# Performance work log

Measured on AMD Instinct MI355X. Metric: run time of the kernel, lower is better.

The kernel has to match this reference:

```python
import jax, jax.numpy as jnp
import numpy as np

PH = PW = 5  # roi_size
EPS = 1e-5


def _conv1x1(x, w, b):
    # x: (B,Cin,H,W), w: (Cout,Cin)
    return jnp.einsum('bchw,oc->bohw', x, w) + b[None, :, None, None]


def _resize_ac(x, oh, ow):
    # F.interpolate bilinear, align_corners=True. x: (B,C,H,W)
    B, C, H, W = x.shape
    ys = jnp.linspace(0.0, H - 1.0, oh)
    xs = jnp.linspace(0.0, W - 1.0, ow)
    y0 = jnp.floor(ys).astype(jnp.int32); y1 = jnp.minimum(y0 + 1, H - 1)
    x0 = jnp.floor(xs).astype(jnp.int32); x1 = jnp.minimum(x0 + 1, W - 1)
    ly = (ys - y0)[:, None]; lx = (xs - x0)[None, :]
    v00 = x[:, :, y0[:, None], x0[None, :]]
    v01 = x[:, :, y0[:, None], x1[None, :]]
    v10 = x[:, :, y1[:, None], x0[None, :]]
    v11 = x[:, :, y1[:, None], x1[None, :]]
    return v00 * (1 - ly) * (1 - lx) + v01 * (1 - ly) * lx + v10 * ly * (1 - lx) + v11 * ly * lx


def _roi_align_one(feat, box):
    # torchvision RoIAlign, spatial_scale=1, sampling_ratio=1, aligned=False
    # feat: (C,H,W), box: (x1,y1,x2,y2)
    C, H, W = feat.shape
    bx1, by1, bx2, by2 = box[0], box[1], box[2], box[3]
    rw = jnp.maximum(bx2 - bx1, 1.0)
    rh = jnp.maximum(by2 - by1, 1.0)
    xs = bx1 + (jnp.arange(PW, dtype=feat.dtype) + 0.5) * (rw / PW)
    ys = by1 + (jnp.arange(PH, dtype=feat.dtype) + 0.5) * (rh / PH)
    yg = jnp.broadcast_to(ys[:, None], (PH, PW))
    xg = jnp.broadcast_to(xs[None, :], (PH, PW))
    valid = (yg >= -1.0) & (yg <= H) & (xg >= -1.0) & (xg <= W)
    y = jnp.clip(yg, 0.0, H - 1.0); x = jnp.clip(xg, 0.0, W - 1.0)
    y0 = jnp.floor(y).astype(jnp.int32); x0 = jnp.floor(x).astype(jnp.int32)
    y1i = jnp.minimum(y0 + 1, H - 1); x1i = jnp.minimum(x0 + 1, W - 1)
    ly = y - y0; lx = x - x0
    v = (feat[:, y0, x0] * (1 - ly) * (1 - lx) + feat[:, y0, x1i] * (1 - ly) * lx
         + feat[:, y1i, x0] * ly * (1 - lx) + feat[:, y1i, x1i] * ly * lx)
    return v * valid  # (C,PH,PW)


def _layernorm(x, w, b):
    mu = jnp.mean(x, -1, keepdims=True)
    var = jnp.var(x, -1, keepdims=True)
    return (x - mu) * jax.lax.rsqrt(var + EPS) * w + b


def setup_inputs() -> dict:
    key = jax.random.key(0)
    ks = jax.random.split(key, 16)
    B, G, NB, HF = 8, 8, 16, 28
    x4 = jax.random.normal(ks[0], (B, 1024, 14, 14), jnp.float32)
    x5 = jax.random.normal(ks[1], (B, 2048, 7, 7), jnp.float32)
    bx = jax.random.uniform(ks[2], (B, NB), minval=0.0, maxval=18.0)
    by = jax.random.uniform(ks[3], (B, NB), minval=0.0, maxval=18.0)
    bw = jax.random.uniform(ks[4], (B, NB), minval=3.0, maxval=10.0)
    bh = jax.random.uniform(ks[5], (B, NB), minval=3.0, maxval=10.0)
    boxes = jnp.stack([bx, by, jnp.minimum(bx + bw, 28.0), jnp.minimum(by + bh, 28.0)], -1)
    group = jax.random.randint(ks[6], (B, G, 2), 0, NB, jnp.int32)
    real_in_num = jnp.full((B,), G, jnp.int32)
    label_s = jax.random.randint(ks[7], (B, G), 0, 6, jnp.int64)
    label_s = jnp.where(jnp.arange(G)[None, :] % 3 == 0, -1, label_s)  # exercise both branches
    skeleton = jax.random.normal(ks[8], (B, G, HF, HF), jnp.float32)
    D = 1536 * PH * PW  # 38400
    return {
        'x4': x4, 'x5': x5, 'boxes': boxes, 'skeleton': skeleton,
        'group': group, 'real_in_num': real_in_num, 'label_s': label_s,
        'conv1_w': jax.random.normal(ks[9], (), jnp.float32) * 0.5,
        'conv1_b': jax.random.normal(ks[10], (), jnp.float32) * 0.1,
        'conv2_w': jax.random.normal(ks[11], (512, 1024), jnp.float32) * 0.03,
        'conv2_b': jnp.zeros((512,), jnp.float32),
        'conv3_w': jax.random.normal(ks[12], (1024, 2048), jnp.float32) * 0.02,
        'conv3_b': jnp.zeros((1024,), jnp.float32),
        'norm1_w': jnp.ones((D,), jnp.float32), 'norm1_b': jnp.zeros((D,), jnp.float32),
        'norm2_w': jnp.ones((512,), jnp.float32), 'norm2_b': jnp.zeros((512,), jnp.float32),
        'fc1_w': jax.random.normal(ks[13], (512, D), jnp.float32) * float(np.sqrt(2.0 / D)),
        'fc1_b': jnp.zeros((512,), jnp.float32),
        'fc2_w': jax.random.normal(ks[14], (6, 512), jnp.float32) * float(np.sqrt(2.0 / 512)),
        'fc2_b': jnp.zeros((6,), jnp.float32),
    }


def reference(x4, x5, boxes, skeleton, group, real_in_num, label_s,
              conv1_w, conv1_b, conv2_w, conv2_b, conv3_w, conv3_b,
              norm1_w, norm1_b, norm2_w, norm2_b, fc1_w, fc1_b, fc2_w, fc2_b):
    B, G = skeleton.shape[0], skeleton.shape[1]
    HF, WF = skeleton.shape[2], skeleton.shape[3]
    # backbone heads: 1x1 conv + bilinear upsample (align_corners=True), concat
    f4 = _resize_ac(_conv1x1(x4, conv2_w, conv2_b), HF, WF)   # (B,512,28,28)
    f5 = _resize_ac(_conv1x1(x5, conv3_w, conv3_b), HF, WF)   # (B,1024,28,28)
    app = jnp.concatenate([f4, f5], axis=1)                   # (B,1536,28,28)
    C = app.shape[1]
    # per-person pose gate: 1x1 conv (scalar on single channel) + sigmoid
    gate = jax.nn.sigmoid(skeleton * conv1_w + conv1_b)       # (B,G,28,28)
    gated = gate[:, :, None] * app[:, None]                   # (B,G,C,28,28)
    use_gate = (label_s != -1)[:, :, None, None, None]
    pose_feature = jnp.where(use_gate, gated, app[:, None])   # (B,G,C,28,28)
    # union box of the two interacting people (get_box_tensor)
    bidx = jnp.arange(B)[:, None]
    b1 = boxes[bidx, group[..., 0]]                           # (B,G,4)
    b2 = boxes[bidx, group[..., 1]]
    ub = jnp.stack([jnp.minimum(b1[..., 0], b2[..., 0]), jnp.minimum(b1[..., 1], b2[..., 1]),
                    jnp.maximum(b1[..., 2], b2[..., 2]), jnp.maximum(b1[..., 3], b2[..., 3])], -1)
    # batched RoIAlign over all N = B*G boxes
    feats = pose_feature.reshape(B * G, C, HF, WF)
    rois = jax.vmap(_roi_align_one)(feats, ub.reshape(B * G, 4))  # (N,C,5,5)
    sk = rois.reshape(B * G, -1)                              # (N,38400)
    sk = jax.nn.relu(_layernorm(sk, norm1_w, norm1_b))
    # dropout(p=0.9) is identity in eval mode
    sk = sk @ fc1_w.T + fc1_b
    sk = _layernorm(sk, norm2_w, norm2_b)
    score = sk @ fc2_w.T + fc2_b                              # (N,6)
    return score
```

## Files before the change

kernel.cpp:

```cpp
#include <hip/hip_runtime.h>
#include <hip/hip_cooperative_groups.h>
#include <math.h>

namespace cg = cooperative_groups;

#define B8   8
#define HW4  196
#define HW5  49
#define HFW  28
#define NPIX 784
#define CAPP 1536
#define D1   38400
#define NR   64

typedef short short8 __attribute__((ext_vector_type(8)));
typedef short short4v __attribute__((ext_vector_type(4)));
typedef float floatx16 __attribute__((ext_vector_type(16)));

__device__ __forceinline__ unsigned short f2bf(float f) {
  unsigned u = __float_as_uint(f);
  u += 0x7FFF + ((u >> 16) & 1);
  return (unsigned short)(u >> 16);
}

struct Params {
  const float *x4, *x5, *boxes, *skel;
  const int *group, *label;
  const float *c1w, *c1b, *w2c, *b2c, *w3c, *b3c;
  const float *n1w, *n1b, *n2w, *n2b, *fw1, *fb1, *fw2, *fb2;
  float* out;
  unsigned short *x4T, *x5T, *sknT;
  float *f4T, *f5T, *tap4w, *tap5w, *descw, *roisP, *stats, *out1;
  int *tap4o, *tap5o, *desco;
};

union SharedU {
  float tile[32 * 201];
  struct {
    unsigned short As[2][4096];
    unsigned short Bs[2][4096];
  } g;
  struct {
    float cw4[16], cw5[16], wgs;
    int co4[16], co5[16];
    float red[8];
  } roi;
  struct {
    float red[8];
    float red2[24];
  } ln;
};

__device__ __forceinline__ void gemm_unit(
    SharedU& sh, const unsigned short* __restrict__ A, const float* __restrict__ Bw,
    float* __restrict__ C, int mt, int nt, int k0, int kchunk,
    int K, int N, int Mvalid) {
  int t = threadIdx.x;
  int wave = t >> 6, lane = t & 63;
  int wm = wave & 1, wn = wave >> 1;
  const unsigned short* Aptr = A + (size_t)(mt * 64) * K + k0;
  const float* Bptr = Bw + (size_t)(nt * 64) * K + k0;
  short8 areg[2];
  float4 breg[4];
  floatx16 acc;
#pragma unroll
  for (int i = 0; i < 16; i++) acc[i] = 0.f;
  int nkb = kchunk >> 6;

#pragma unroll
  for (int i = 0; i < 2; i++) {
    int e = t + i * 256;
    areg[i] = *(const short8*)(Aptr + (size_t)(e >> 3) * K + (e & 7) * 8);
  }
#pragma unroll
  for (int i = 0; i < 4; i++) {
    int e = t + i * 256;
    breg[i] = *(const float4*)(Bptr + (size_t)(e >> 4) * K + (e & 15) * 4);
  }
#pragma unroll
  for (int i = 0; i < 2; i++) {
    int e = t + i * 256;
    int m = e >> 3, ko = e & 7;
    *(short8*)&sh.g.As[0][ko * 512 + ((m ^ ko)) * 8] = areg[i];
  }
#pragma unroll
  for (int i = 0; i < 4; i++) {
    int e = t + i * 256;
    short4v v;
    v[0] = (short)f2bf(breg[i].x); v[1] = (short)f2bf(breg[i].y);
    v[2] = (short)f2bf(breg[i].z); v[3] = (short)f2bf(breg[i].w);
    int ko = (e & 15) >> 1, half = (e & 15) & 1, n = e >> 4;
    *(short4v*)&sh.g.Bs[0][ko * 512 + ((n ^ ko)) * 8 + half * 4] = v;
  }
  __syncthreads();

  for (int kb = 0; kb < nkb; kb++) {
    int buf = kb & 1;
    bool more = (kb + 1) < nkb;
    if (more) {
      int kof = (kb + 1) * 64;
#pragma unroll
      for (int i = 0; i < 2; i++) {
        int e = t + i * 256;
        areg[i] = *(const short8*)(Aptr + (size_t)(e >> 3) * K + kof + (e & 7) * 8);
      }
#pragma unroll
      for (int i = 0; i < 4; i++) {
        int e = t + i * 256;
        breg[i] = *(const float4*)(Bptr + (size_t)(e >> 4) * K + kof + (e & 15) * 4);
      }
    }
#pragma unroll
    for (int s = 0; s < 4; s++) {
      int ko = 2 * s + (lane >> 5);
      int am = wm * 32 + (lane & 31);
      int bn = wn * 32 + (lane & 31);
      short8 af = *(const short8*)&sh.g.As[buf][ko * 512 + ((am ^ ko)) * 8];
      short8 bf = *(const short8*)&sh.g.Bs[buf][ko * 512 + ((bn ^ ko)) * 8];
      acc = __builtin_amdgcn_mfma_f32_32x32x16_bf16(af, bf, acc, 0, 0, 0);
    }
    __syncthreads();
    if (more) {
      int nb2 = 1 - buf;
#pragma unroll
      for (int i = 0; i < 2; i++) {
        int e = t + i * 256;
        int m = e >> 3, ko = e & 7;
        *(short8*)&sh.g.As[nb2][ko * 512 + ((m ^ ko)) * 8] = areg[i];
      }
#pragma unroll
      for (int i = 0; i < 4; i++) {
        int e = t + i * 256;
        short4v v;
        v[0] = (short)f2bf(breg[i].x); v[1] = (short)f2bf(breg[i].y);
        v[2] = (short)f2bf(breg[i].z); v[3] = (short)f2bf(breg[i].w);
        int ko = (e & 15) >> 1, half = (e & 15) & 1, n = e >> 4;
        *(short4v*)&sh.g.Bs[nb2][ko * 512 + ((n ^ ko)) * 8 + half * 4] = v;
      }
      __syncthreads();
    }
  }

  int col = nt * 64 + wn * 32 + (lane & 31);
  int rbase = mt * 64 + wm * 32 + 4 * (lane >> 5);
#pragma unroll
  for (int reg = 0; reg < 16; reg++) {
    int row = rbase + (reg & 3) + 8 * (reg >> 2);
    if (row < Mvalid) atomicAdd(&C[(size_t)row * N + col], acc[reg]);
  }
}

__device__ __forceinline__ float gate_val(const float* sk, int yy, int xx,
                                          float c1w, float c1b, bool use) {
  if (!use) return 1.f;
  float z = sk[yy * HFW + xx] * c1w + c1b;
  return 1.f / (1.f + expf(-z));
}

__device__ void run_phase(const Params& p, int phase, SharedU& sh) {
  int bid = blockIdx.x, t = threadIdx.x, gb = gridDim.x;
  int gtid = bid * 256 + t;
  int nth = gb * 256;

  if (phase == 0) {
    float4 z4 = make_float4(0.f, 0.f, 0.f, 0.f);
    for (int i = gtid; i < 319488; i += nth) ((float4*)p.f4T)[i] = z4;
    for (int i = gtid; i < 8192; i += nth) ((float4*)p.out1)[i] = z4;
    if (gtid < 128) p.stats[gtid] = 0.f;

    for (int u = bid; u < 836; u += gb) {
      __syncthreads();
      if (u < 256) {
        int b = u >> 5, cc = u & 31;
        for (int i = t; i < 32 * HW4; i += 256) {
          int c = i / HW4, hw = i - c * HW4;
          sh.tile[c * 201 + hw] = p.x4[((size_t)(b * 1024 + cc * 32 + c)) * HW4 + hw];
        }
        __syncthreads();
        for (int i = t; i < HW4 * 32; i += 256) {
          int hw = i >> 5, c = i & 31;
          p.x4T[((size_t)(b * HW4 + hw)) * 1024 + cc * 32 + c] = f2bf(sh.tile[c * 201 + hw]);
        }
      } else if (u < 768) {
        int u2 = u - 256;
        int b = u2 >> 6, cc = u2 & 63;
        for (int i = t; i < 32 * HW5; i += 256) {
          int c = i / HW5, hw = i - c * HW5;
          sh.tile[c * 51 + hw] = p.x5[((size_t)(b * 2048 + cc * 32 + c)) * HW5 + hw];
        }
        __syncthreads();
        for (int i = t; i < HW5 * 32; i += 256) {
          int hw = i >> 5, c = i & 31;
          p.x5T[((size_t)(b * HW5 + hw)) * 2048 + cc * 32 + c] = f2bf(sh.tile[c * 51 + hw]);
        }
      } else if (u < 832) {
        int bg = u - 768;
        if (t < 25) {
          int b = bg >> 3;
          int i1 = p.group[bg * 2 + 0], i2 = p.group[bg * 2 + 1];
          const float* bb1 = p.boxes + (size_t)(b * 16 + i1) * 4;
          const float* bb2 = p.boxes + (size_t)(b * 16 + i2) * 4;
          float ux1 = fminf(bb1[0], bb2[0]);
          float uy1 = fminf(bb1[1], bb2[1]);
          float ux2 = fmaxf(bb1[2], bb2[2]);
          float uy2 = fmaxf(bb1[3], bb2[3]);
          float rw = fmaxf(ux2 - ux1, 1.0f), rh = fmaxf(uy2 - uy1, 1.0f);
          int iy = t / 5, ix = t % 5;
          float sy = uy1 + (iy + 0.5f) * (rh * 0.2f);
          float sx = ux1 + (ix + 0.5f) * (rw * 0.2f);
          float valid = (sy >= -1.0f && sy <= 28.0f && sx >= -1.0f && sx <= 28.0f) ? 1.f : 0.f;
          float y = fminf(fmaxf(sy, 0.f), 27.f);
          float x = fminf(fmaxf(sx, 0.f), 27.f);
          int y0 = (int)floorf(y), x0 = (int)floorf(x);
          int y1 = min(y0 + 1, 27), x1 = min(x0 + 1, 27);
          float ly = y - (float)y0, lx = x - (float)x0;
          bool use = (p.label[bg] != -1);
          float c1w = p.c1w[0], c1b = p.c1b[0];
          const float* sk = p.skel + (size_t)bg * NPIX;
          int idx = (bg * 25 + t) * 4;
          p.descw[idx + 0] = (1.f - ly) * (1.f - lx) * valid * gate_val(sk, y0, x0, c1w, c1b, use);
          p.descw[idx + 1] = (1.f - ly) * lx * valid * gate_val(sk, y0, x1, c1w, c1b, use);
          p.descw[idx + 2] = ly * (1.f - lx) * valid * gate_val(sk, y1, x0, c1w, c1b, use);
          p.descw[idx + 3] = ly * lx * valid * gate_val(sk, y1, x1, c1w, c1b, use);
          p.desco[idx + 0] = y0 * HFW + x0;
          p.desco[idx + 1] = y0 * HFW + x1;
          p.desco[idx + 2] = y1 * HFW + x0;
          p.desco[idx + 3] = y1 * HFW + x1;
        }
      } else {
        int pix = (u - 832) * 196 + t;
        if (t < 196) {
          int y = pix / HFW, x = pix % HFW;
          {
            float sy = y * (13.0f / 27.0f), sx = x * (13.0f / 27.0f);
            int y0 = (int)sy, x0 = (int)sx;
            int y1 = min(y0 + 1, 13), x1 = min(x0 + 1, 13);
            float ly = sy - y0, lx = sx - x0;
            p.tap4o[pix * 4 + 0] = y0 * 14 + x0; p.tap4w[pix * 4 + 0] = (1.f - ly) * (1.f - lx);
            p.tap4o[pix * 4 + 1] = y0 * 14 + x1; p.tap4w[pix * 4 + 1] = (1.f - ly) * lx;
            p.tap4o[pix * 4 + 2] = y1 * 14 + x0; p.tap4w[pix * 4 + 2] = ly * (1.f - lx);
            p.tap4o[pix * 4 + 3] = y1 * 14 + x1; p.tap4w[pix * 4 + 3] = ly * lx;
          }
          {
            float sy = y * (6.0f / 27.0f), sx = x * (6.0f / 27.0f);
            int y0 = (int)sy, x0 = (int)sx;
            int y1 = min(y0 + 1, 6), x1 = min(x0 + 1, 6);
            float ly = sy - y0, lx = sx - x0;
            p.tap5o[pix * 4 + 0] = y0 * 7 + x0; p.tap5w[pix * 4 + 0] = (1.f - ly) * (1.f - lx);
            p.tap5o[pix * 4 + 1] = y0 * 7 + x1; p.tap5w[pix * 4 + 1] = (1.f - ly) * lx;
            p.tap5o[pix * 4 + 2] = y1 * 7 + x0; p.tap5w[pix * 4 + 2] = ly * (1.f - lx);
            p.tap5o[pix * 4 + 3] = y1 * 7 + x1; p.tap5w[pix * 4 + 3] = ly * lx;
          }
        }
      }
    }

  } else if (phase == 1) {
    for (int u = bid; u < 1696; u += gb) {
      __syncthreads();
      if (u < 800) {
        int mt = u % 25, r = u / 25;
        int nt = r & 7, sp = r >> 3;
        gemm_unit(sh, p.x4T, p.w2c, p.f4T, mt, nt, sp * 256, 256, 1024, 512, 1568);
      } else {
        int u2 = u - 800;
        int mt = u2 % 7, r = u2 / 7;
        int nt = r & 15, sp = r >> 4;
        gemm_unit(sh, p.x5T, p.w3c, p.f5T, mt, nt, sp * 256, 256, 2048, 1024, 392);
      }
    }

  } else if (phase == 2) {
    for (int u = bid; u < 1600; u += gb) {
      __syncthreads();
      int pp = u % 25, bg = u / 25, b = bg >> 3;
      int di = (bg * 25 + pp) * 4;
      if (t < 16) {
        int i = t >> 2, j = t & 3;
        float wg = p.descw[di + i];
        int pix = p.desco[di + i];
        sh.roi.cw4[t] = wg * p.tap4w[pix * 4 + j];
        sh.roi.co4[t] = (b * HW4 + p.tap4o[pix * 4 + j]) * 512;
        sh.roi.cw5[t] = wg * p.tap5w[pix * 4 + j];
        sh.roi.co5[t] = (b * HW5 + p.tap5o[pix * 4 + j]) * 1024;
      }
      if (t == 16) sh.roi.wgs = p.descw[di] + p.descw[di + 1] + p.descw[di + 2] + p.descw[di + 3];
      __syncthreads();
      float w4r[16], w5r[16];
      int o4r[16], o5r[16];
      float wg = sh.roi.wgs;
#pragma unroll
      for (int i = 0; i < 16; i++) {
        w4r[i] = sh.roi.cw4[i]; o4r[i] = sh.roi.co4[i];
        w5r[i] = sh.roi.cw5[i]; o5r[i] = sh.roi.co5[i];
      }
      float ls = 0.f, ls2 = 0.f;
      float* outp = p.roisP + (size_t)(bg * 25 + pp) * CAPP;
      for (int c = t; c < 512; c += 256) {
        float acc = wg * p.b2c[c];
#pragma unroll
        for (int i = 0; i < 16; i++) acc = fmaf(w4r[i], p.f4T[o4r[i] + c], acc);
        outp[c] = acc;
        ls += acc; ls2 = fmaf(acc, acc, ls2);
      }
      for (int c = t; c < 1024; c += 256) {
        float acc = wg * p.b3c[c];
#pragma unroll
        for (int i = 0; i < 16; i++) acc = fmaf(w5r[i], p.f5T[o5r[i] + c], acc);
        outp[512 + c] = acc;
        ls += acc; ls2 = fmaf(acc, acc, ls2);
      }
      for (int off = 32; off; off >>= 1) {
        ls += __shfl_down(ls, off);
        ls2 += __shfl_down(ls2, off);
      }
      int wv = t >> 6;
      if ((t & 63) == 0) { sh.roi.red[wv] = ls; sh.roi.red[4 + wv] = ls2; }
      __syncthreads();
      if (t == 0) {
        atomicAdd(&p.stats[bg * 2 + 0], sh.roi.red[0] + sh.roi.red[1] + sh.roi.red[2] + sh.roi.red[3]);
        atomicAdd(&p.stats[bg * 2 + 1], sh.roi.red[4] + sh.roi.red[5] + sh.roi.red[6] + sh.roi.red[7]);
      }
    }

  } else if (phase == 3) {
    for (int o = gtid; o < NR * D1; o += nth) {
      int r = o / D1;
      int k = o - r * D1;
      unsigned c = (unsigned)k / 25u;
      unsigned pp = (unsigned)k - c * 25u;
      float x = p.roisP[((size_t)(r * 25 + pp)) * CAPP + c];
      float S = p.stats[r * 2], S2 = p.stats[r * 2 + 1];
      float mu = S * (1.f / D1);
      float var = S2 * (1.f / D1) - mu * mu;
      float rs = rsqrtf(var + 1e-5f);
      float v = fmaf((x - mu) * rs, p.n1w[k], p.n1b[k]);
      p.sknT[o] = f2bf(fmaxf(v, 0.f));
    }

  } else if (phase == 4) {
    for (int u = bid; u < 960; u += gb) {
      __syncthreads();
      int nt = u & 7, sp = u >> 3;
      gemm_unit(sh, p.sknT, p.fw1, p.out1, 0, nt, sp * 320, 320, 38400, 512, 64);
    }

  } else {
    for (int r = bid; r < NR; r += gb) {
      __syncthreads();
      int j1 = t, j2 = t + 256;
      float v1 = p.out1[r * 512 + j1] + p.fb1[j1];
      float v2 = p.out1[r * 512 + j2] + p.fb1[j2];
      float s = v1 + v2, s2 = v1 * v1 + v2 * v2;
      for (int off = 32; off; off >>= 1) {
        s += __shfl_down(s, off);
        s2 += __shfl_down(s2, off);
      }
      int wv = t >> 6;
      if ((t & 63) == 0) { sh.ln.red[wv] = s; sh.ln.red[4 + wv] = s2; }
      __syncthreads();
      float S = sh.ln.red[0] + sh.ln.red[1] + sh.ln.red[2] + sh.ln.red[3];
      float S2 = sh.ln.red[4] + sh.ln.red[5] + sh.ln.red[6] + sh.ln.red[7];
      float mu = S / 512.f;
      float var = S2 / 512.f - mu * mu;
      float rs = rsqrtf(var + 1e-5f);
      float n1v = fmaf((v1 - mu) * rs, p.n2w[j1], p.n2b[j1]);
      float n2v = fmaf((v2 - mu) * rs, p.n2w[j2], p.n2b[j2]);
      float pm[6];
#pragma unroll
      for (int m = 0; m < 6; m++)
        pm[m] = n1v * p.fw2[m * 512 + j1] + n2v * p.fw2[m * 512 + j2];
#pragma unroll
      for (int m = 0; m < 6; m++)
        for (int off = 32; off; off >>= 1) pm[m] += __shfl_down(pm[m], off);
      if ((t & 63) == 0) {
#pragma unroll
        for (int m = 0; m < 6; m++) sh.ln.red2[wv * 6 + m] = pm[m];
      }
      __syncthreads();
      if (t < 6)
        p.out[r * 6 + t] = sh.ln.red2[t] + sh.ln.red2[6 + t] + sh.ln.red2[12 + t] +
                           sh.ln.red2[18 + t] + p.fb2[t];
    }
  }
}

__global__ __launch_bounds__(256, 4) void mega_kernel(Params p) {
  cg::grid_group grid = cg::this_grid();
  __shared__ SharedU sh;
  run_phase(p, 0, sh);
  __threadfence(); grid.sync();
  run_phase(p, 1, sh);
  __threadfence(); grid.sync();
  run_phase(p, 2, sh);
  __threadfence(); grid.sync();
  run_phase(p, 3, sh);
  __threadfence(); grid.sync();
  run_phase(p, 4, sh);
  __threadfence(); grid.sync();
  run_phase(p, 5, sh);
}

__global__ __launch_bounds__(256, 4) void phase_kernel(Params p, int phase) {
  __shared__ SharedU sh;
  run_phase(p, phase, sh);
}

extern "C" void kernel_launch(void* const* d_in, const int* in_sizes, int n_in,
                              void* d_out, int out_size, void* d_ws, size_t ws_size,
                              hipStream_t stream) {
  Params p;
  p.x4    = (const float*)d_in[0];
  p.x5    = (const float*)d_in[1];
  p.boxes = (const float*)d_in[2];
  p.skel  = (const float*)d_in[3];
  p.group = (const int*)d_in[4];
  p.label = (const int*)d_in[6];
  p.c1w   = (const float*)d_in[7];
  p.c1b   = (const float*)d_in[8];
  p.w2c   = (const float*)d_in[9];
  p.b2c   = (const float*)d_in[10];
  p.w3c   = (const float*)d_in[11];
  p.b3c   = (const float*)d_in[12];
  p.n1w   = (const float*)d_in[13];
  p.n1b   = (const float*)d_in[14];
  p.n2w   = (const float*)d_in[15];
  p.n2b   = (const float*)d_in[16];
  p.fw1   = (const float*)d_in[17];
  p.fb1   = (const float*)d_in[18];
  p.fw2   = (const float*)d_in[19];
  p.fb2   = (const float*)d_in[20];
  p.out   = (float*)d_out;

  float* ws = (float*)d_ws;
  p.x4T   = (unsigned short*)ws;
  p.x5T   = (unsigned short*)(ws + 819200);
  p.f4T   = ws + 1277952;
  p.f5T   = ws + 2097152;
  p.tap4w = ws + 2555904;
  p.tap4o = (int*)(ws + 2559040);
  p.tap5w = ws + 2562176;
  p.tap5o = (int*)(ws + 2565312);
  p.descw = ws + 2568448;
  p.desco = (int*)(ws + 2574848);
  p.roisP = ws + 2581248;
  p.stats = ws + 5038848;
  p.sknT  = (unsigned short*)(ws + 5038976);
  p.out1  = ws + 6267776;

  int nb = 0;
  hipError_t e = hipOccupancyMaxActiveBlocksPerMultiprocessor(
      &nb, (const void*)mega_kernel, 256, 0);
  int grid = (e == hipSuccess) ? nb * 256 : 0;

  if (grid >= 768) {
    if (grid > 1024) grid = 1024;
    void* args[] = { (void*)&p };
    hipLaunchCooperativeKernel((const void*)mega_kernel, dim3(grid), dim3(256),
                               args, 0, stream);
  } else {
    phase_kernel<<<836, 256, 0, stream>>>(p, 0);
    phase_kernel<<<1696, 256, 0, stream>>>(p, 1);
    phase_kernel<<<1600, 256, 0, stream>>>(p, 2);
    phase_kernel<<<9600, 256, 0, stream>>>(p, 3);
    phase_kernel<<<960, 256, 0, stream>>>(p, 4);
    phase_kernel<<<64, 256, 0, stream>>>(p, 5);
  }
}
```

Before: 257.0 us.

## Drop cooperative megakernel; stage LayerNorm transpose through shared memory

Removes the cooperative-launch mega kernel with grid syncs and always launches six separate phase kernels. Phase 3 (LayerNorm1 + ReLU + bf16 transpose) now works per (row, 256-channel chunk): it loads the 25x256 slab coalesced into a padded shared tile, then writes the transposed output contiguously. The aim is to replace strided global gathers with coalesced loads and to avoid the cost of grid-wide barriers. In exchange it pays for extra kernel launches. It also assumes the shared union has a `tile` member large enough for 25x257 floats.

```diff
diff --git a/kernel.cpp b/kernel.cpp
--- a/kernel.cpp
+++ b/kernel.cpp
@@ -1,8 +1,5 @@
 #include <hip/hip_runtime.h>
-#include <hip/hip_cooperative_groups.h>
 #include <math.h>
-
-namespace cg = cooperative_groups;
 
 #define B8   8
 #define HW4  196
@@ -324,18 +321,29 @@
     }
 
   } else if (phase == 3) {
-    for (int o = gtid; o < NR * D1; o += nth) {
-      int r = o / D1;
-      int k = o - r * D1;
-      unsigned c = (unsigned)k / 25u;
-      unsigned pp = (unsigned)k - c * 25u;
-      float x = p.roisP[((size_t)(r * 25 + pp)) * CAPP + c];
+    for (int u = bid; u < 384; u += gb) {
+      __syncthreads();
+      int r = u / 6, ch = u - r * 6;
+      int c0 = ch * 256;
       float S = p.stats[r * 2], S2 = p.stats[r * 2 + 1];
       float mu = S * (1.f / D1);
       float var = S2 * (1.f / D1) - mu * mu;
       float rs = rsqrtf(var + 1e-5f);
-      float v = fmaf((x - mu) * rs, p.n1w[k], p.n1b[k]);
-      p.sknT[o] = f2bf(fmaxf(v, 0.f));
+      const float* rp = p.roisP + (size_t)r * 25 * CAPP + c0;
+#pragma unroll
+      for (int pp = 0; pp < 25; pp++)
+        sh.tile[pp * 257 + t] = rp[(size_t)pp * CAPP + t];
+      __syncthreads();
+      unsigned short* op = p.sknT + (size_t)r * D1 + c0 * 25;
+      const float* wv = p.n1w + c0 * 25;
+      const float* bv = p.n1b + c0 * 25;
+      for (int j = t; j < 6400; j += 256) {
+        unsigned cc = (unsigned)j / 25u;
+        unsigned pp = (unsigned)j - cc * 25u;
+        float x = sh.tile[pp * 257 + cc];
+        float v = fmaf((x - mu) * rs, wv[j], bv[j]);
+        op[j] = f2bf(fmaxf(v, 0.f));
+      }
     }
 
   } else if (phase == 4) {
@@ -383,22 +391,6 @@
                            sh.ln.red2[18 + t] + p.fb2[t];
     }
   }
-}
-
-__global__ __launch_bounds__(256, 4) void mega_kernel(Params p) {
-  cg::grid_group grid = cg::this_grid();
-  __shared__ SharedU sh;
-  run_phase(p, 0, sh);
-  __threadfence(); grid.sync();
-  run_phase(p, 1, sh);
-  __threadfence(); grid.sync();
-  run_phase(p, 2, sh);
-  __threadfence(); grid.sync();
-  run_phase(p, 3, sh);
-  __threadfence(); grid.sync();
-  run_phase(p, 4, sh);
-  __threadfence(); grid.sync();
-  run_phase(p, 5, sh);
 }
 
 __global__ __launch_bounds__(256, 4) void phase_kernel(Params p, int phase) {
@@ -448,22 +440,10 @@
   p.sknT  = (unsigned short*)(ws + 5038976);
   p.out1  = ws + 6267776;
 
-  int nb = 0;
-  hipError_t e = hipOccupancyMaxActiveBlocksPerMultiprocessor(
-      &nb, (const void*)mega_kernel, 256, 0);
-  int grid = (e == hipSuccess) ? nb * 256 : 0;
-
-  if (grid >= 768) {
-    if (grid > 1024) grid = 1024;
-    void* args[] = { (void*)&p };
-    hipLaunchCooperativeKernel((const void*)mega_kernel, dim3(grid), dim3(256),
-                               args, 0, stream);
-  } else {
-    phase_kernel<<<836, 256, 0, stream>>>(p, 0);
-    phase_kernel<<<1696, 256, 0, stream>>>(p, 1);
-    phase_kernel<<<1600, 256, 0, stream>>>(p, 2);
-    phase_kernel<<<9600, 256, 0, stream>>>(p, 3);
-    phase_kernel<<<960, 256, 0, stream>>>(p, 4);
-    phase_kernel<<<64, 256, 0, stream>>>(p, 5);
-  }
-}
+  phase_kernel<<<836,  256, 0, stream>>>(p, 0);
+  phase_kernel<<<1696, 256, 0, stream>>>(p, 1);
+  phase_kernel<<<1600, 256, 0, stream>>>(p, 2);
+  phase_kernel<<<384,  256, 0, stream>>>(p, 3);
+  phase_kernel<<<960,  256, 0, stream>>>(p, 4);
+  phase_kernel<<<64,   256, 0, stream>>>(p, 5);
+}
```

Measured after the change: 246.8 us. -4.0%, faster.
